# Kernel optimization log

Hardware: AMD Instinct MI355X
Metric: run time of the kernel (lower is better)

Reference implementation:

```python
import jax, jax.numpy as jnp
import numpy as np

B, S, D = 2, 2048, 2048
H, Dh = 16, 128  # qkv_features = H*Dh = 2048
NEG = -1e10


def setup_inputs() -> dict:
    key = jax.random.key(0)
    k1, k2, k3 = jax.random.split(key, 3)
    x = jax.random.normal(k1, (B, S, D), dtype=jnp.float32)
    # variance_scaling(1.0, 'fan_in', 'normal') ~ std = 1/sqrt(fan_in)
    Wqkv = jax.random.normal(k2, (D, 3 * H * Dh), dtype=jnp.float32) / np.sqrt(D)
    bqkv = jnp.zeros((3 * H * Dh,), dtype=jnp.float32)
    Wout = jax.random.normal(k3, (H * Dh, D), dtype=jnp.float32) / np.sqrt(H * Dh)
    bout = jnp.zeros((D,), dtype=jnp.float32)
    return {"x": x, "Wqkv": Wqkv, "bqkv": bqkv, "Wout": Wout, "bout": bout}


def reference(x, Wqkv, bqkv, Wout, bout):
    b, s, _ = x.shape
    # fused QKV projection
    qkv = x @ Wqkv + bqkv                                   # [B, S, 3*H*Dh]
    qkv = qkv.reshape(b, s, 3, H, Dh).transpose(2, 0, 3, 1, 4)  # [3, B, H, S, Dh]
    q, k, v = qkv[0], qkv[1], qkv[2]
    scale = 1.0 / jnp.sqrt(jnp.asarray(Dh, dtype=x.dtype))
    # Each query chunk attends to the full key sequence with a causal mask,
    # which is mathematically full causal attention.
    scores = jnp.einsum('bhqd,bhkd->bhqk', q, k) * scale    # [B, H, S, S]
    causal = jnp.arange(s)[None, :] <= jnp.arange(s)[:, None]  # k <= q
    scores = jnp.where(causal[None, None, :, :], scores, NEG)
    weights = jax.nn.softmax(scores, axis=-1)
    out = jnp.einsum('bhqk,bhkd->bhqd', weights, v)         # [B, H, S, Dh]
    out = out.transpose(0, 2, 1, 3).reshape(b, s, H * Dh)
    return out @ Wout + bout
```

## Files before the change

kernel.cpp:

```cpp
#include <hip/hip_runtime.h>


typedef unsigned short u16;
typedef __attribute__((ext_vector_type(8))) short bf16x8;
typedef __attribute__((ext_vector_type(4))) float f32x4;

#define MFMA(a, b, c) __builtin_amdgcn_mfma_f32_16x16x32_bf16((a), (b), (c), 0, 0, 0)

__device__ __forceinline__ u16 f2bf(float f) {
    unsigned u = __builtin_bit_cast(unsigned, f);
    u += 0x7fffu + ((u >> 16) & 1u);
    return (u16)(u >> 16);
}

__device__ __forceinline__ void gload16(const void* g, void* l) {
    __builtin_amdgcn_global_load_lds(
        (const __attribute__((address_space(1))) void*)g,
        (__attribute__((address_space(3))) void*)l, 16, 0, 0);
}


__global__ __launch_bounds__(256) void k_cast(const float* __restrict__ src,
                                              u16* __restrict__ dst, int n4) {
    int i = blockIdx.x * 256 + threadIdx.x;
    if (i >= n4) return;
    float4 a = ((const float4*)src)[i];
    ushort4 r;
    r.x = f2bf(a.x); r.y = f2bf(a.y); r.z = f2bf(a.z); r.w = f2bf(a.w);
    ((ushort4*)dst)[i] = r;
}

__global__ __launch_bounds__(256) void k_castT(const float* __restrict__ src,
                                               u16* __restrict__ dst, int rows, int cols) {
    __shared__ float t[32][33];
    int c0 = blockIdx.x * 32, r0 = blockIdx.y * 32;
    int tx = threadIdx.x, ty = threadIdx.y;
#pragma unroll
    for (int i = 0; i < 4; ++i)
        t[ty + 8 * i][tx] = src[(size_t)(r0 + ty + 8 * i) * cols + (c0 + tx)];
    __syncthreads();
#pragma unroll
    for (int i = 0; i < 4; ++i)
        dst[(size_t)(c0 + ty + 8 * i) * rows + (r0 + tx)] = f2bf(t[tx][ty + 8 * i]);
}


template <int K>
__device__ __forceinline__ void gemm_core(const u16* __restrict__ A,
                                          const u16* __restrict__ BT,
                                          int m0, int n0,
                                          f32x4 (&acc)[4][4],
                                          u16* As, u16* Bs) {
    const int tid = threadIdx.x, wave = tid >> 6, lane = tid & 63;
    const int wr = (wave >> 1) * 64, wc = (wave & 1) * 64;
    for (int k0 = 0; k0 < K; k0 += 32) {
        __syncthreads();
#pragma unroll
        for (int i = 0; i < 2; ++i) {
            int cb = (i * 4 + wave) * 64;
            int c = cb + lane;
            int row = c >> 2, kk = (c & 3) * 8;
            gload16(A + (size_t)(m0 + row) * K + k0 + kk, As + cb * 8);
            gload16(BT + (size_t)(n0 + row) * K + k0 + kk, Bs + cb * 8);
        }
        __syncthreads();
        bf16x8 a[4], b[4];
#pragma unroll
        for (int m = 0; m < 4; ++m)
            a[m] = *(const bf16x8*)(As + (wr + m * 16 + (lane & 15)) * 32 + (lane >> 4) * 8);
#pragma unroll
        for (int n = 0; n < 4; ++n)
            b[n] = *(const bf16x8*)(Bs + (wc + n * 16 + (lane & 15)) * 32 + (lane >> 4) * 8);
        __builtin_amdgcn_s_setprio(1);
#pragma unroll
        for (int m = 0; m < 4; ++m)
#pragma unroll
            for (int n = 0; n < 4; ++n)
                acc[m][n] = MFMA(a[m], b[n], acc[m][n]);
        __builtin_amdgcn_s_setprio(0);
    }
}

__global__ __launch_bounds__(256) void k_gemm_qkv(const u16* __restrict__ A,
                                                  const u16* __restrict__ BT,
                                                  const float* __restrict__ bias,
                                                  u16* __restrict__ q,
                                                  u16* __restrict__ kbuf,
                                                  u16* __restrict__ vT) {
    __shared__ __align__(16) u16 As[128 * 32];
    __shared__ __align__(16) u16 Bs[128 * 32];
    f32x4 acc[4][4] = {};
    const int orig = blockIdx.y * 48 + blockIdx.x;
    const int nb = (orig & 7) * 192 + (orig >> 3);
    const int m0 = (nb / 48) * 128, n0 = (nb % 48) * 128;
    gemm_core<2048>(A, BT, m0, n0, acc, As, Bs);

    const int tid = threadIdx.x, wave = tid >> 6, lane = tid & 63;
    const int wr = (wave >> 1) * 64, wc = (wave & 1) * 64;
    const int t = n0 >> 11;
#pragma unroll
    for (int m = 0; m < 4; ++m)
#pragma unroll
        for (int n = 0; n < 4; ++n)
#pragma unroll
            for (int j = 0; j < 4; ++j) {
                int gr = m0 + wr + m * 16 + (lane >> 4) * 4 + j;
                int gc = n0 + wc + n * 16 + (lane & 15);
                float val = acc[m][n][j] + bias[gc];
                int bb = gr >> 11, s = gr & 2047;
                int rem = gc & 2047, h = rem >> 7, d = rem & 127;
                u16 bv = f2bf(val);
                if (t == 0)
                    q[((size_t)(bb * 16 + h) * 2048 + s) * 128 + d] = bv;
                else if (t == 1)
                    kbuf[((size_t)(bb * 16 + h) * 2048 + s) * 128 + d] = bv;
                else
                    vT[((size_t)(bb * 16 + h) * 128 + d) * 2048 + s] = bv;
            }
}

__global__ __launch_bounds__(256) void k_gemm_out(const u16* __restrict__ A,
                                                  const u16* __restrict__ BT,
                                                  const float* __restrict__ bias,
                                                  float* __restrict__ out) {
    __shared__ __align__(16) u16 As[128 * 32];
    __shared__ __align__(16) u16 Bs[128 * 32];
    f32x4 acc[4][4] = {};
    const int orig = blockIdx.y * 16 + blockIdx.x;
    const int nb = (orig & 7) * 64 + (orig >> 3);
    const int m0 = (nb / 16) * 128, n0 = (nb % 16) * 128;
    gemm_core<2048>(A, BT, m0, n0, acc, As, Bs);

    const int tid = threadIdx.x, wave = tid >> 6, lane = tid & 63;
    const int wr = (wave >> 1) * 64, wc = (wave & 1) * 64;
#pragma unroll
    for (int m = 0; m < 4; ++m)
#pragma unroll
        for (int n = 0; n < 4; ++n)
#pragma unroll
            for (int j = 0; j < 4; ++j) {
                int gr = m0 + wr + m * 16 + (lane >> 4) * 4 + j;
                int gc = n0 + wc + n * 16 + (lane & 15);
                out[(size_t)gr * 2048 + gc] = acc[m][n][j] + bias[gc];
            }
}

__global__ __launch_bounds__(512) void k_attn(const u16* __restrict__ q,
                                              const u16* __restrict__ k,
                                              const u16* __restrict__ vT,
                                              u16* __restrict__ o) {
    __shared__ __align__(16) u16 KsA[2 * 64 * 128];
    __shared__ __align__(16) u16 VsA[2 * 128 * 64];
    __shared__ __align__(16) u16 PsA[8 * 16 * 64];
    char* ksB = (char*)KsA;
    char* vsB = (char*)VsA;

    const int tid = threadIdx.x, wave = tid >> 6, lane = tid & 63;
    char* psB = (char*)PsA + wave * 2048;

    const int lin = blockIdx.x;
    const int dd = (lin & 7) * 32 + (lin >> 3);
    const int head = dd >> 3, pair = dd & 7;

    const u16* qh = q + (size_t)head * 2048 * 128;
    const u16* kh = k + (size_t)head * 2048 * 128;
    const u16* vh = vT + (size_t)head * 128 * 2048;
    const int bb = head >> 4, hh = head & 15;
    const float qscale = 0.1275293562566334f;
    const float MFIX = 20.f;

    bf16x8 ones;
#pragma unroll
    for (int e = 0; e < 8; ++e) ones[e] = (short)0x3F80;

    auto stage = [&](int kv0, int bufsel) {
        char* kd = ksB + bufsel * 16384;
        char* vd = vsB + bufsel * 16384;
#pragma unroll
        for (int i = 0; i < 2; ++i) {
            int cb = (i * 8 + wave) * 64;
            int d = (cb + lane) * 16;
            int r = d >> 8;
            int co = (d & 255) ^ ((r & 7) << 4);
            gload16(kh + (size_t)(kv0 + r) * 128 + (co >> 1), kd + cb * 16);
        }
#pragma unroll
        for (int i = 0; i < 2; ++i) {
            int cb = (i * 8 + wave) * 64;
            int d = (cb + lane) * 16;
            int vr = d >> 7;
            int co = (d & 127) ^ ((vr & 7) << 4);
            gload16(vh + (size_t)vr * 2048 + kv0 + (co >> 1), vd + cb * 16);
        }
    };

#pragma unroll 1
    for (int qsel = 0; qsel < 2; ++qsel) {
        const int qi = qsel ? (15 - pair) : pair;
        const int q0 = qi * 128;
        const int ntile = 2 * qi + 2;

        bf16x8 qf[4];
        const int qr = q0 + wave * 16 + (lane & 15);
#pragma unroll
        for (int kt = 0; kt < 4; ++kt)
            qf[kt] = *(const bf16x8*)(qh + (size_t)qr * 128 + kt * 32 + (lane >> 4) * 8);

        f32x4 o_acc[8] = {};
        f32x4 l_r = {};

        stage(0, 0);
        int buf = 0;

#pragma unroll 1
        for (int t = 0; t < ntile; ++t) {
            const int kv0 = t * 64;
            if (t + 1 < ntile) {
                stage(kv0 + 64, buf ^ 1);
                asm volatile("s_waitcnt vmcnt(4)" ::: "memory");
            } else {
                asm volatile("s_waitcnt vmcnt(0)" ::: "memory");
            }
            __builtin_amdgcn_s_barrier();
            char* kb_ = ksB + buf * 16384;
            char* vb_ = vsB + buf * 16384;

            f32x4 s_acc[4] = {};
            __builtin_amdgcn_s_setprio(1);
#pragma unroll
            for (int c = 0; c < 4; ++c) {
                int row = c * 16 + (lane & 15);
#pragma unroll
                for (int kt = 0; kt < 4; ++kt) {
                    bf16x8 kbf = *(const bf16x8*)(kb_ +
                        ((row * 256 + kt * 64 + (lane >> 4) * 16) ^ ((row & 7) << 4)));
                    s_acc[c] = MFMA(qf[kt], kbf, s_acc[c]);
                }
            }
            __builtin_amdgcn_s_setprio(0);

            const bool maskblk = (kv0 + 64 > q0 + wave * 16);
#pragma unroll
            for (int j = 0; j < 4; ++j) {
                int qg = q0 + wave * 16 + (lane >> 4) * 4 + j;
#pragma unroll
                for (int c = 0; c < 4; ++c) {
                    float sv = fmaf(s_acc[c][j], qscale, -MFIX);
                    if (maskblk && (kv0 + c * 16 + (lane & 15)) > qg) sv = -1e30f;
                    s_acc[c][j] = exp2f(sv);
                }
            }

#pragma unroll
            for (int c = 0; c < 4; ++c)
#pragma unroll
                for (int j = 0; j < 4; ++j) {
                    int row = (lane >> 4) * 4 + j;
                    *(u16*)(psB + ((row * 128 + (c * 16 + (lane & 15)) * 2) ^ ((row & 7) << 4)))
                        = f2bf(s_acc[c][j]);
                }
            bf16x8 pf[2];
#pragma unroll
            for (int kt = 0; kt < 2; ++kt) {
                int row2 = lane & 15;
                pf[kt] = *(const bf16x8*)(psB +
                    ((row2 * 128 + kt * 64 + (lane >> 4) * 16) ^ ((row2 & 7) << 4)));
            }

            __builtin_amdgcn_s_setprio(1);
            l_r = MFMA(pf[0], ones, l_r);
            l_r = MFMA(pf[1], ones, l_r);
#pragma unroll
            for (int c2 = 0; c2 < 8; ++c2) {
#pragma unroll
                for (int kt = 0; kt < 2; ++kt) {
                    int row = c2 * 16 + (lane & 15);
                    bf16x8 vf = *(const bf16x8*)(vb_ +
                        ((row * 128 + kt * 64 + (lane >> 4) * 16) ^ ((row & 7) << 4)));
                    o_acc[c2] = MFMA(pf[kt], vf, o_acc[c2]);
                }
            }
            __builtin_amdgcn_s_setprio(0);

            __builtin_amdgcn_s_barrier();
            buf ^= 1;
        }

        float linv[4];
#pragma unroll
        for (int j = 0; j < 4; ++j) linv[j] = 1.0f / l_r[j];
#pragma unroll
        for (int c2 = 0; c2 < 8; ++c2)
#pragma unroll
            for (int j = 0; j < 4; ++j) {
                int qg = q0 + wave * 16 + (lane >> 4) * 4 + j;
                int d2 = c2 * 16 + (lane & 15);
                o[((size_t)(bb * 2048 + qg)) * 2048 + hh * 128 + d2]
                    = f2bf(o_acc[c2][j] * linv[j]);
            }
    }
}


extern "C" void kernel_launch(void* const* d_in, const int* in_sizes, int n_in,
                              void* d_out, int out_size, void* d_ws, size_t ws_size,
                              hipStream_t stream) {
    const float* x    = (const float*)d_in[0];
    const float* Wqkv = (const float*)d_in[1];
    const float* bqkv = (const float*)d_in[2];
    const float* Wout = (const float*)d_in[3];
    const float* bout = (const float*)d_in[4];
    float* out = (float*)d_out;

    char* ws = (char*)d_ws;
    const size_t SZ = 16777216;
    u16* q   = (u16*)(ws);
    u16* kb  = (u16*)(ws + SZ);
    u16* ao  = (u16*)(ws + 2 * SZ);
    u16* vT  = (u16*)(ws + 3 * SZ);
    u16* xb  = (u16*)(ws + 4 * SZ);
    u16* WqT = (u16*)(ws + 5 * SZ);
    u16* WoT = (u16*)(ws + 5 * SZ + 25165824);

    k_cast<<<dim3(8192), dim3(256), 0, stream>>>(x, xb, 2097152);
    k_castT<<<dim3(192, 64), dim3(32, 8), 0, stream>>>(Wqkv, WqT, 2048, 6144);
    k_castT<<<dim3(64, 64), dim3(32, 8), 0, stream>>>(Wout, WoT, 2048, 2048);
    k_gemm_qkv<<<dim3(48, 32), dim3(256), 0, stream>>>(xb, WqT, bqkv, q, kb, vT);
    k_attn<<<dim3(256), dim3(512), 0, stream>>>(q, kb, vT, ao);
    k_gemm_out<<<dim3(16, 32), dim3(256), 0, stream>>>(ao, WoT, bout, out);
}
```

Before: 305.5 us.

## Write V row-major from QKV GEMM, transpose separately, skip fully masked attention tiles

```diff
diff --git a/kernel.cpp b/kernel.cpp
--- a/kernel.cpp
+++ b/kernel.cpp
@@ -42,6 +42,23 @@
 #pragma unroll
     for (int i = 0; i < 4; ++i)
         dst[(size_t)(c0 + ty + 8 * i) * rows + (r0 + tx)] = f2bf(t[tx][ty + 8 * i]);
+}
+
+__global__ __launch_bounds__(256) void k_transv(const u16* __restrict__ v,
+                                                u16* __restrict__ vT) {
+    __shared__ u16 t[32][33];
+    int head = blockIdx.z;
+    int s0 = blockIdx.x * 32, d0 = blockIdx.y * 32;
+    const u16* vp = v + (size_t)head * 2048 * 128;
+    u16* op = vT + (size_t)head * 128 * 2048;
+    int tx = threadIdx.x, ty = threadIdx.y;
+#pragma unroll
+    for (int i = 0; i < 4; ++i)
+        t[ty + 8 * i][tx] = vp[(size_t)(s0 + ty + 8 * i) * 128 + d0 + tx];
+    __syncthreads();
+#pragma unroll
+    for (int i = 0; i < 4; ++i)
+        op[(size_t)(d0 + ty + 8 * i) * 2048 + (s0 + tx)] = t[tx][ty + 8 * i];
 }
 
 
@@ -86,7 +103,7 @@
                                                   const float* __restrict__ bias,
                                                   u16* __restrict__ q,
                                                   u16* __restrict__ kbuf,
-                                                  u16* __restrict__ vT) {
+                                                  u16* __restrict__ v) {
     __shared__ __align__(16) u16 As[128 * 32];
     __shared__ __align__(16) u16 Bs[128 * 32];
     f32x4 acc[4][4] = {};
@@ -98,6 +115,7 @@
     const int tid = threadIdx.x, wave = tid >> 6, lane = tid & 63;
     const int wr = (wave >> 1) * 64, wc = (wave & 1) * 64;
     const int t = n0 >> 11;
+    u16* dst = (t == 0) ? q : (t == 1) ? kbuf : v;
 #pragma unroll
     for (int m = 0; m < 4; ++m)
 #pragma unroll
@@ -109,13 +127,7 @@
                 float val = acc[m][n][j] + bias[gc];
                 int bb = gr >> 11, s = gr & 2047;
                 int rem = gc & 2047, h = rem >> 7, d = rem & 127;
-                u16 bv = f2bf(val);
-                if (t == 0)
-                    q[((size_t)(bb * 16 + h) * 2048 + s) * 128 + d] = bv;
-                else if (t == 1)
-                    kbuf[((size_t)(bb * 16 + h) * 2048 + s) * 128 + d] = bv;
-                else
-                    vT[((size_t)(bb * 16 + h) * 128 + d) * 2048 + s] = bv;
+                dst[((size_t)(bb * 16 + h) * 2048 + s) * 128 + d] = f2bf(val);
             }
 }
 
@@ -225,62 +237,64 @@
             char* kb_ = ksB + buf * 16384;
             char* vb_ = vsB + buf * 16384;
 
-            f32x4 s_acc[4] = {};
-            __builtin_amdgcn_s_setprio(1);
-#pragma unroll
-            for (int c = 0; c < 4; ++c) {
-                int row = c * 16 + (lane & 15);
-#pragma unroll
-                for (int kt = 0; kt < 4; ++kt) {
-                    bf16x8 kbf = *(const bf16x8*)(kb_ +
-                        ((row * 256 + kt * 64 + (lane >> 4) * 16) ^ ((row & 7) << 4)));
-                    s_acc[c] = MFMA(qf[kt], kbf, s_acc[c]);
+            if (kv0 <= q0 + wave * 16 + 15) {
+                f32x4 s_acc[4] = {};
+                __builtin_amdgcn_s_setprio(1);
+#pragma unroll
+                for (int c = 0; c < 4; ++c) {
+                    int row = c * 16 + (lane & 15);
+#pragma unroll
+                    for (int kt = 0; kt < 4; ++kt) {
+                        bf16x8 kbf = *(const bf16x8*)(kb_ +
+                            ((row * 256 + kt * 64 + (lane >> 4) * 16) ^ ((row & 7) << 4)));
+                        s_acc[c] = MFMA(qf[kt], kbf, s_acc[c]);
+                    }
                 }
-            }
-            __builtin_amdgcn_s_setprio(0);
-
-            const bool maskblk = (kv0 + 64 > q0 + wave * 16);
-#pragma unroll
-            for (int j = 0; j < 4; ++j) {
-                int qg = q0 + wave * 16 + (lane >> 4) * 4 + j;
-#pragma unroll
-                for (int c = 0; c < 4; ++c) {
-                    float sv = fmaf(s_acc[c][j], qscale, -MFIX);
-                    if (maskblk && (kv0 + c * 16 + (lane & 15)) > qg) sv = -1e30f;
-                    s_acc[c][j] = exp2f(sv);
+                __builtin_amdgcn_s_setprio(0);
+
+                const bool maskblk = (kv0 + 64 > q0 + wave * 16);
+#pragma unroll
+                for (int j = 0; j < 4; ++j) {
+                    int qg = q0 + wave * 16 + (lane >> 4) * 4 + j;
+#pragma unroll
+                    for (int c = 0; c < 4; ++c) {
+                        float sv = fmaf(s_acc[c][j], qscale, -MFIX);
+                        if (maskblk && (kv0 + c * 16 + (lane & 15)) > qg) sv = -1e30f;
+                        s_acc[c][j] = exp2f(sv);
+                    }
                 }
-            }
-
-#pragma unroll
-            for (int c = 0; c < 4; ++c)
-#pragma unroll
-                for (int j = 0; j < 4; ++j) {
-                    int row = (lane >> 4) * 4 + j;
-                    *(u16*)(psB + ((row * 128 + (c * 16 + (lane & 15)) * 2) ^ ((row & 7) << 4)))
-                        = f2bf(s_acc[c][j]);
+
+#pragma unroll
+                for (int c = 0; c < 4; ++c)
+#pragma unroll
+                    for (int j = 0; j < 4; ++j) {
+                        int row = (lane >> 4) * 4 + j;
+                        *(u16*)(psB + ((row * 128 + (c * 16 + (lane & 15)) * 2) ^ ((row & 7) << 4)))
+                            = f2bf(s_acc[c][j]);
+                    }
+                bf16x8 pf[2];
+#pragma unroll
+                for (int kt = 0; kt < 2; ++kt) {
+                    int row2 = lane & 15;
+                    pf[kt] = *(const bf16x8*)(psB +
+                        ((row2 * 128 + kt * 64 + (lane >> 4) * 16) ^ ((row2 & 7) << 4)));
                 }
-            bf16x8 pf[2];
-#pragma unroll
-            for (int kt = 0; kt < 2; ++kt) {
-                int row2 = lane & 15;
-                pf[kt] = *(const bf16x8*)(psB +
-                    ((row2 * 128 + kt * 64 + (lane >> 4) * 16) ^ ((row2 & 7) << 4)));
-            }
-
-            __builtin_amdgcn_s_setprio(1);
-            l_r = MFMA(pf[0], ones, l_r);
-            l_r = MFMA(pf[1], ones, l_r);
-#pragma unroll
-            for (int c2 = 0; c2 < 8; ++c2) {
-#pragma unroll
-                for (int kt = 0; kt < 2; ++kt) {
-                    int row = c2 * 16 + (lane & 15);
-                    bf16x8 vf = *(const bf16x8*)(vb_ +
-                        ((row * 128 + kt * 64 + (lane >> 4) * 16) ^ ((row & 7) << 4)));
-                    o_acc[c2] = MFMA(pf[kt], vf, o_acc[c2]);
+
+                __builtin_amdgcn_s_setprio(1);
+                l_r = MFMA(pf[0], ones, l_r);
+                l_r = MFMA(pf[1], ones, l_r);
+#pragma unroll
+                for (int c2 = 0; c2 < 8; ++c2) {
+#pragma unroll
+                    for (int kt = 0; kt < 2; ++kt) {
+                        int row = c2 * 16 + (lane & 15);
+                        bf16x8 vf = *(const bf16x8*)(vb_ +
+                            ((row * 128 + kt * 64 + (lane >> 4) * 16) ^ ((row & 7) << 4)));
+                        o_acc[c2] = MFMA(pf[kt], vf, o_acc[c2]);
+                    }
                 }
-            }
-            __builtin_amdgcn_s_setprio(0);
+                __builtin_amdgcn_s_setprio(0);
+            }
 
             __builtin_amdgcn_s_barrier();
             buf ^= 1;
@@ -316,8 +330,9 @@
     const size_t SZ = 16777216;
     u16* q   = (u16*)(ws);
     u16* kb  = (u16*)(ws + SZ);
-    u16* ao  = (u16*)(ws + 2 * SZ);
+    u16* v   = (u16*)(ws + 2 * SZ);
     u16* vT  = (u16*)(ws + 3 * SZ);
+    u16* ao  = v;
     u16* xb  = (u16*)(ws + 4 * SZ);
     u16* WqT = (u16*)(ws + 5 * SZ);
     u16* WoT = (u16*)(ws + 5 * SZ + 25165824);
@@ -325,7 +340,8 @@
     k_cast<<<dim3(8192), dim3(256), 0, stream>>>(x, xb, 2097152);
     k_castT<<<dim3(192, 64), dim3(32, 8), 0, stream>>>(Wqkv, WqT, 2048, 6144);
     k_castT<<<dim3(64, 64), dim3(32, 8), 0, stream>>>(Wout, WoT, 2048, 2048);
-    k_gemm_qkv<<<dim3(48, 32), dim3(256), 0, stream>>>(xb, WqT, bqkv, q, kb, vT);
+    k_gemm_qkv<<<dim3(48, 32), dim3(256), 0, stream>>>(xb, WqT, bqkv, q, kb, v);
+    k_transv<<<dim3(64, 4, 32), dim3(32, 8), 0, stream>>>(v, vT);
     k_attn<<<dim3(256), dim3(512), 0, stream>>>(q, kb, vT, ao);
     k_gemm_out<<<dim3(16, 32), dim3(256), 0, stream>>>(ao, WoT, bout, out);
 }
```

Result: faster. 280.9 us (-8.1%).
